# Kernel optimization log

Hardware: AMD Instinct MI355X
Metric: run time of the kernel (lower is better)

## Reference

```python
import jax, jax.numpy as jnp
import numpy as np

N = 100000   # nodes
E = 1600000  # edges
B = 64       # graphs
NI, EI, GI = 64, 32, 32   # node_in, edge_in, global_in
NO, EO, GO = 32, 32, 32   # node_out, edge_out, global_out
H = 3                     # attention heads
NEG_SLOPE = 0.2


def setup_inputs() -> dict:
    key = jax.random.key(0)
    ks = jax.random.split(key, 20)
    s = 0.1
    return {
        # graph data
        "x": jax.random.normal(ks[0], (N, NI), jnp.float32),
        "edge_attr": jax.random.normal(ks[1], (E, EI), jnp.float32),
        "glob": jax.random.normal(ks[2], (B, GI), jnp.float32),
        # edge_mlp: Lin(node_in+edge_in, edge_out)
        "W_edge": jax.random.normal(ks[3], (NI + EI, EO), jnp.float32) * s,
        "b_edge": jax.random.normal(ks[4], (EO,), jnp.float32) * s,
        # GATv2Conv params (heads=3, edge_dim=EO)
        "W_l": jax.random.normal(ks[5], (NI, H * NO), jnp.float32) * s,
        "b_l": jax.random.normal(ks[6], (H * NO,), jnp.float32) * s,
        "W_r": jax.random.normal(ks[7], (NI, H * NO), jnp.float32) * s,
        "b_r": jax.random.normal(ks[8], (H * NO,), jnp.float32) * s,
        "W_e": jax.random.normal(ks[9], (EO, H * NO), jnp.float32) * s,   # lin_edge (no bias)
        "att": jax.random.normal(ks[10], (H, NO), jnp.float32) * s,
        "bias_gat": jax.random.normal(ks[11], (H * NO,), jnp.float32) * s,
        # node_mlp_2: Lin(node_out*3 + global_in, node_out)
        "W_n2": jax.random.normal(ks[12], (H * NO + GI, NO), jnp.float32) * s,
        "b_n2": jax.random.normal(ks[13], (NO,), jnp.float32) * s,
        # global_mlp: Lin(global_in + node_out, global_out)
        "W_g": jax.random.normal(ks[14], (GI + NO, GO), jnp.float32) * s,
        "b_g": jax.random.normal(ks[15], (GO,), jnp.float32) * s,
        # int inputs
        "edge_index": jax.random.randint(ks[16], (2, E), 0, N, jnp.int32),
        "batch": jnp.sort(jax.random.randint(ks[17], (N,), 0, B, jnp.int32)),
    }


def reference(x, edge_attr, glob, W_edge, b_edge, W_l, b_l, W_r, b_r, W_e,
              att, bias_gat, W_n2, b_n2, W_g, b_g, edge_index, batch):
    src, dst = edge_index[0], edge_index[1]

    # --- edge model: relu(Lin([x[src], edge_attr])) ---
    e = jax.nn.relu(jnp.concatenate([x[src], edge_attr], axis=1) @ W_edge + b_edge)  # [E, EO]

    # --- node model: GATv2Conv(heads=3, edge_dim=EO), concat heads ---
    xl = (x @ W_l + b_l).reshape(N, H, NO)   # source transform
    xr = (x @ W_r + b_r).reshape(N, H, NO)   # target transform
    m = xl[src] + xr[dst] + (e @ W_e).reshape(E, H, NO)          # [E,H,NO]
    logits = (jax.nn.leaky_relu(m, NEG_SLOPE) * att).sum(-1)     # [E,H]
    # segment softmax over incoming edges of each target node
    mx = jax.ops.segment_max(logits, dst, num_segments=N)        # [N,H]
    ex = jnp.exp(logits - mx[dst])
    den = jax.ops.segment_sum(ex, dst, num_segments=N)           # [N,H]
    alpha = ex / den[dst]                                        # [E,H]
    msg = (alpha[..., None] * xl[src]).reshape(E, H * NO)
    gat_out = jax.ops.segment_sum(msg, dst, num_segments=N) + bias_gat  # [N, H*NO]
    x_new = jax.nn.relu(jnp.concatenate([gat_out, glob[batch]], axis=1) @ W_n2 + b_n2)  # [N,NO]

    # --- global model: relu(Lin([glob, scatter_mean(x_new, batch)])) ---
    cnt = jax.ops.segment_sum(jnp.ones((N,), x.dtype), batch, num_segments=B)
    mean = jax.ops.segment_sum(x_new, batch, num_segments=B) / jnp.maximum(cnt, 1.0)[:, None]
    u_new = jax.nn.relu(jnp.concatenate([glob, mean], axis=1) @ W_g + b_g)  # [B,GO]

    return x_new, e, u_new
```

## Files before the change

### kernel.cpp

```cpp
#include <hip/hip_runtime.h>

#define N_NODES 100000
#define N_EDGES 1600000
#define NB 64
#define NI 64
#define EI 32
#define GI 32
#define NO 32
#define EO 32
#define GO 32
#define HH 3
#define HNO 96
#define NEG 0.2f
#define SCAN_BLKS 98
#define SCAT_BLKS 1024
#define KE_BLKS 2048

__global__ __launch_bounds__(256) void kA_node(
    const float* __restrict__ x,
    const float* __restrict__ W_l, const float* __restrict__ b_l,
    const float* __restrict__ W_r, const float* __restrict__ b_r,
    const float* __restrict__ W_edge, const float* __restrict__ b_edge,
    float* __restrict__ xl, float* __restrict__ xr, float* __restrict__ pre_e,
    int niters)
{
    __shared__ float sWl[NI * HNO];
    __shared__ float sWr[NI * HNO];
    __shared__ float sWp[NI * 32];
    __shared__ float sx[64 * NI];
    int t = threadIdx.x;
    for (int f = t; f < NI * HNO; f += 256) { sWl[f] = W_l[f]; sWr[f] = W_r[f]; }
    for (int f = t; f < NI * 32; f += 256) sWp[f] = W_edge[f];
    __syncthreads();
    int k = t & 31, g = t >> 5;
    float bl0 = b_l[k], bl1 = b_l[k + 32], bl2 = b_l[k + 64];
    float br0 = b_r[k], br1 = b_r[k + 32], br2 = b_r[k + 64];
    float bpe = b_edge[k];
    const long NX = (long)N_NODES * NI;
    for (int it = 0; it < niters; ++it) {
        long nb = ((long)blockIdx.x + (long)it * gridDim.x) * 64;
        long base = nb * NI;
        for (int f = t; f < 64 * NI; f += 256) {
            long idx = base + f;
            sx[f] = x[idx < NX ? idx : 0];
        }
        __syncthreads();
        float aL0[8], aL1[8], aL2[8], aR0[8], aR1[8], aR2[8], aP[8];
        #pragma unroll
        for (int m = 0; m < 8; ++m) {
            aL0[m] = bl0; aL1[m] = bl1; aL2[m] = bl2;
            aR0[m] = br0; aR1[m] = br1; aR2[m] = br2;
            aP[m] = bpe;
        }
        const float* sxg = &sx[g * 8 * NI];
        for (int i = 0; i < NI; ++i) {
            float wl0 = sWl[i * HNO + k], wl1 = sWl[i * HNO + 32 + k], wl2 = sWl[i * HNO + 64 + k];
            float wr0 = sWr[i * HNO + k], wr1 = sWr[i * HNO + 32 + k], wr2 = sWr[i * HNO + 64 + k];
            float wp  = sWp[i * 32 + k];
            #pragma unroll
            for (int m = 0; m < 8; ++m) {
                float xv = sxg[m * NI + i];
                aL0[m] += xv * wl0; aL1[m] += xv * wl1; aL2[m] += xv * wl2;
                aR0[m] += xv * wr0; aR1[m] += xv * wr1; aR2[m] += xv * wr2;
                aP[m]  += xv * wp;
            }
        }
        #pragma unroll
        for (int m = 0; m < 8; ++m) {
            long n = nb + g * 8 + m;
            if (n < N_NODES) {
                xl[n * HNO + k]      = aL0[m];
                xl[n * HNO + 32 + k] = aL1[m];
                xl[n * HNO + 64 + k] = aL2[m];
                xr[n * HNO + k]      = aR0[m];
                xr[n * HNO + 32 + k] = aR1[m];
                xr[n * HNO + 64 + k] = aR2[m];
                pre_e[n * 32 + k]    = aP[m];
            }
        }
        __syncthreads();
    }
}

__global__ __launch_bounds__(256) void k_hist(const int* __restrict__ eidx, int* __restrict__ cnt)
{
    long i = (long)blockIdx.x * 256 + threadIdx.x;
    long stride = (long)gridDim.x * 256;
    for (; i < N_EDGES; i += stride)
        atomicAdd(&cnt[eidx[N_EDGES + i]], 1);
}

__global__ __launch_bounds__(1024) void k_scan1(const int* __restrict__ cnt, int* __restrict__ bsum)
{
    __shared__ int s[1024];
    int i = blockIdx.x * 1024 + threadIdx.x;
    s[threadIdx.x] = (i < N_NODES) ? cnt[i] : 0;
    for (int o = 512; o > 0; o >>= 1) {
        __syncthreads();
        if (threadIdx.x < o) s[threadIdx.x] += s[threadIdx.x + o];
    }
    if (threadIdx.x == 0) bsum[blockIdx.x] = s[0];
}

__global__ __launch_bounds__(128) void k_scan2(int* __restrict__ bsum)
{
    __shared__ int s[128];
    int v = (threadIdx.x < SCAN_BLKS) ? bsum[threadIdx.x] : 0;
    s[threadIdx.x] = v;
    for (int o = 1; o < 128; o <<= 1) {
        __syncthreads();
        int a = (threadIdx.x >= o) ? s[threadIdx.x - o] : 0;
        __syncthreads();
        s[threadIdx.x] += a;
    }
    if (threadIdx.x < SCAN_BLKS) bsum[threadIdx.x] = s[threadIdx.x] - v;
}

__global__ __launch_bounds__(1024) void k_scan3(const int* __restrict__ cnt,
                                                const int* __restrict__ bsum,
                                                int* __restrict__ off, int* __restrict__ cursor)
{
    __shared__ int s[1024];
    int i = blockIdx.x * 1024 + threadIdx.x;
    int v = (i < N_NODES) ? cnt[i] : 0;
    s[threadIdx.x] = v;
    for (int o = 1; o < 1024; o <<= 1) {
        __syncthreads();
        int a = (threadIdx.x >= o) ? s[threadIdx.x - o] : 0;
        __syncthreads();
        s[threadIdx.x] += a;
    }
    int excl = bsum[blockIdx.x] + s[threadIdx.x] - v;
    if (i < N_NODES) {
        off[i] = excl; cursor[i] = excl;
        if (i == N_NODES - 1) off[N_NODES] = excl + v;
    }
}

__global__ __launch_bounds__(256) void k_scat_ke(
    const int* __restrict__ eidx, int* __restrict__ cursor, int2* __restrict__ ep,
    const float* __restrict__ pre_e, const float* __restrict__ ea,
    const float* __restrict__ W_edge, float* __restrict__ e_out)
{
    __shared__ float sW2[32 * 32];
    __shared__ float sEa[8][32];
    int t = threadIdx.x;
    if (blockIdx.x < SCAT_BLKS) {
        long i = (long)blockIdx.x * 256 + t;
        long stride = (long)SCAT_BLKS * 256;
        for (; i < N_EDGES; i += stride) {
            int s = eidx[i];
            int d = eidx[N_EDGES + i];
            int pos = atomicAdd(&cursor[d], 1);
            ep[pos] = make_int2((int)i, s);
        }
    } else {
        int bid = blockIdx.x - SCAT_BLKS;
        for (int f = t; f < 32 * 32; f += 256) sW2[f] = W_edge[64 * 32 + f];
        __syncthreads();
        int k = t & 31, gid = t >> 5;
        const int niters = (N_EDGES + KE_BLKS * 8 - 1) / (KE_BLKS * 8);
        for (int it = 0; it < niters; ++it) {
            long e = ((long)bid + (long)it * KE_BLKS) * 8 + gid;
            bool valid = (e < N_EDGES);
            long ec = valid ? e : 0;
            int s = eidx[ec];
            float acc = pre_e[(long)s * 32 + k];
            sEa[gid][k] = ea[ec * EI + k];
            #pragma unroll 8
            for (int i = 0; i < 32; ++i) acc += sEa[gid][i] * sW2[i * 32 + k];
            if (valid) e_out[ec * EO + k] = fmaxf(acc, 0.f);
        }
    }
}

__global__ __launch_bounds__(256) void kF(
    const float* __restrict__ eo_in, const float* __restrict__ W_e,
    const float* __restrict__ att,
    const float* __restrict__ xl, const float* __restrict__ xr,
    const int2* __restrict__ ep, const int* __restrict__ off,
    const float* __restrict__ bias_gat,
    float* __restrict__ g_out, int niters)
{
    __shared__ float sWe[32 * 96];
    __shared__ float2 sEo2[8][32];
    int t = threadIdx.x;
    for (int f = t; f < 32 * 96; f += 256) sWe[f] = W_e[f];
    __syncthreads();
    int k = t & 31, gid = t >> 5;
    float at0 = att[k], at1 = att[32 + k], at2 = att[64 + k];
    float bg0 = bias_gat[k], bg1 = bias_gat[32 + k], bg2 = bias_gat[64 + k];
    for (int it = 0; it < niters; ++it) {
        long n = ((long)blockIdx.x + (long)it * gridDim.x) * 8 + gid;
        if (n >= N_NODES) continue;
        int lo = off[n], hi = off[n + 1];
        float xr0 = xr[n * HNO + k];
        float xr1 = xr[n * HNO + 32 + k];
        float xr2 = xr[n * HNO + 64 + k];
        float a0 = 0.f, a1 = 0.f, a2 = 0.f;
        float d0 = 0.f, d1 = 0.f, d2 = 0.f;
        int deg = hi - lo;
        int steps = (deg + 1) >> 1;
        int eA = 0, sA = 0, eB = 0, sB = 0;
        int eA1 = 0, sA1 = 0, eB1 = 0, sB1 = 0;
        float eoAc = 0.f, eoBc = 0.f;
        float xlA0 = 0.f, xlA1 = 0.f, xlA2 = 0.f, xlB0 = 0.f, xlB1 = 0.f, xlB2 = 0.f;
        if (steps > 0) {
            int2 q = ep[lo]; eA = q.x; sA = q.y;
            if (lo + 1 < hi) { int2 r = ep[lo + 1]; eB = r.x; sB = r.y; }
            eoAc = eo_in[(long)eA * EO + k];
            eoBc = eo_in[(long)eB * EO + k];
            xlA0 = xl[(long)sA * HNO + k]; xlA1 = xl[(long)sA * HNO + 32 + k]; xlA2 = xl[(long)sA * HNO + 64 + k];
            xlB0 = xl[(long)sB * HNO + k]; xlB1 = xl[(long)sB * HNO + 32 + k]; xlB2 = xl[(long)sB * HNO + 64 + k];
            if (lo + 2 < hi) { int2 q1 = ep[lo + 2]; eA1 = q1.x; sA1 = q1.y; }
            if (lo + 3 < hi) { int2 r1 = ep[lo + 3]; eB1 = r1.x; sB1 = r1.y; }
        }
        for (int st = 0; st < steps; ++st) {
            float eoA_n = eo_in[(long)eA1 * EO + k];
            float eoB_n = eo_in[(long)eB1 * EO + k];
            float xlA0n = xl[(long)sA1 * HNO + k], xlA1n = xl[(long)sA1 * HNO + 32 + k], xlA2n = xl[(long)sA1 * HNO + 64 + k];
            float xlB0n = xl[(long)sB1 * HNO + k], xlB1n = xl[(long)sB1 * HNO + 32 + k], xlB2n = xl[(long)sB1 * HNO + 64 + k];
            int eA2 = 0, sA2 = 0, eB2 = 0, sB2 = 0;
            int pA2 = lo + 2 * st + 4;
            if (pA2 < hi)     { int2 q2 = ep[pA2];     eA2 = q2.x; sA2 = q2.y; }
            if (pA2 + 1 < hi) { int2 r2 = ep[pA2 + 1]; eB2 = r2.x; sB2 = r2.y; }
            sEo2[gid][k] = make_float2(eoAc, eoBc);
            float hA0 = xlA0 + xr0, hA1 = xlA1 + xr1, hA2 = xlA2 + xr2;
            float hB0 = xlB0 + xr0, hB1 = xlB1 + xr1, hB2 = xlB2 + xr2;
            #pragma unroll 8
            for (int i = 0; i < 32; ++i) {
                float2 ov = sEo2[gid][i];
                float w0 = sWe[i * 96 + k], w1 = sWe[i * 96 + 32 + k], w2v = sWe[i * 96 + 64 + k];
                hA0 += ov.x * w0; hA1 += ov.x * w1; hA2 += ov.x * w2v;
                hB0 += ov.y * w0; hB1 += ov.y * w1; hB2 += ov.y * w2v;
            }
            float pA0 = (hA0 > 0.f ? hA0 : NEG * hA0) * at0;
            float pA1 = (hA1 > 0.f ? hA1 : NEG * hA1) * at1;
            float pA2v = (hA2 > 0.f ? hA2 : NEG * hA2) * at2;
            float pB0 = (hB0 > 0.f ? hB0 : NEG * hB0) * at0;
            float pB1 = (hB1 > 0.f ? hB1 : NEG * hB1) * at1;
            float pB2 = (hB2 > 0.f ? hB2 : NEG * hB2) * at2;
            #pragma unroll
            for (int m = 1; m <= 16; m <<= 1) {
                pA0 += __shfl_xor(pA0, m, 32); pA1 += __shfl_xor(pA1, m, 32); pA2v += __shfl_xor(pA2v, m, 32);
                pB0 += __shfl_xor(pB0, m, 32); pB1 += __shfl_xor(pB1, m, 32); pB2 += __shfl_xor(pB2, m, 32);
            }
            bool okB = (lo + 2 * st + 1) < hi;
            float exA0 = __expf(pA0), exA1 = __expf(pA1), exA2 = __expf(pA2v);
            float exB0 = 0.f, exB1 = 0.f, exB2 = 0.f;
            if (okB) { exB0 = __expf(pB0); exB1 = __expf(pB1); exB2 = __expf(pB2); }
            a0 += exA0 * xlA0; a1 += exA1 * xlA1; a2 += exA2 * xlA2;
            a0 += exB0 * xlB0; a1 += exB1 * xlB1; a2 += exB2 * xlB2;
            d0 += exA0 + exB0; d1 += exA1 + exB1; d2 += exA2 + exB2;
            eA = eA1; sA = sA1; eB = eB1; sB = sB1;
            eA1 = eA2; sA1 = sA2; eB1 = eB2; sB1 = sB2;
            eoAc = eoA_n; eoBc = eoB_n;
            xlA0 = xlA0n; xlA1 = xlA1n; xlA2 = xlA2n;
            xlB0 = xlB0n; xlB1 = xlB1n; xlB2 = xlB2n;
        }
        g_out[n * HNO + k]      = (d0 > 0.f ? a0 / d0 : 0.f) + bg0;
        g_out[n * HNO + 32 + k] = (d1 > 0.f ? a1 / d1 : 0.f) + bg1;
        g_out[n * HNO + 64 + k] = (d2 > 0.f ? a2 / d2 : 0.f) + bg2;
    }
}

__global__ __launch_bounds__(256) void k2_node_out(
    const float* __restrict__ g, const float* __restrict__ glob,
    const int* __restrict__ batch, const float* __restrict__ W_n2,
    const float* __restrict__ b_n2, float* __restrict__ x_new, int niters)
{
    __shared__ float sW[128 * 32];
    __shared__ float sIn[8][128];
    int t = threadIdx.x;
    for (int f = t; f < 128 * 32; f += 256) sW[f] = W_n2[f];
    __syncthreads();
    int k = t & 31, ni = t >> 5;
    float bn = b_n2[k];
    for (int it = 0; it < niters; ++it) {
        long n = ((long)blockIdx.x + (long)it * gridDim.x) * 8 + ni;
        long nc = (n < N_NODES) ? n : 0;
        #pragma unroll
        for (int r = 0; r < 3; ++r) {
            int j = r * 32 + k;
            sIn[ni][j] = g[nc * HNO + j];
        }
        sIn[ni][96 + k] = glob[(long)batch[nc] * GI + k];
        __syncthreads();
        float acc = bn;
        #pragma unroll 8
        for (int i = 0; i < 128; ++i) acc += sIn[ni][i] * sW[i * 32 + k];
        if (n < N_NODES) x_new[n * NO + k] = fmaxf(acc, 0.f);
        __syncthreads();
    }
}

__device__ __forceinline__ int lower_bound_dev(const int* __restrict__ a, int n, int v) {
    int lo = 0, hi = n;
    while (lo < hi) { int mid = (lo + hi) >> 1; if (a[mid] < v) lo = mid + 1; else hi = mid; }
    return lo;
}

__global__ __launch_bounds__(256) void k3_global(
    const float* __restrict__ x_new, const int* __restrict__ batch,
    const float* __restrict__ glob, const float* __restrict__ W_g,
    const float* __restrict__ b_g, float* __restrict__ u_new)
{
    __shared__ int s_lo, s_hi;
    __shared__ float s_part[8][32];
    __shared__ float s_mean[32];
    int g = blockIdx.x;
    if (threadIdx.x == 0) {
        s_lo = lower_bound_dev(batch, N_NODES, g);
        s_hi = lower_bound_dev(batch, N_NODES, g + 1);
    }
    __syncthreads();
    int lo = s_lo, hi = s_hi;
    int k = threadIdx.x & 31, c = threadIdx.x >> 5;
    float acc = 0.f;
    for (long n = lo + c; n < hi; n += 8) acc += x_new[n * NO + k];
    s_part[c][k] = acc;
    __syncthreads();
    if (threadIdx.x < 32) {
        float s = 0.f;
        #pragma unroll
        for (int c2 = 0; c2 < 8; ++c2) s += s_part[c2][k];
        int cnt = hi - lo;
        s_mean[k] = s / (float)(cnt > 0 ? cnt : 1);
    }
    __syncthreads();
    if (threadIdx.x < 32) {
        float acc2 = b_g[k];
        #pragma unroll
        for (int i = 0; i < 32; ++i) acc2 += glob[g * GI + i] * W_g[i * GO + k];
        #pragma unroll
        for (int i = 0; i < 32; ++i) acc2 += s_mean[i] * W_g[(32 + i) * GO + k];
        u_new[g * GO + k] = fmaxf(acc2, 0.f);
    }
}

extern "C" void kernel_launch(void* const* d_in, const int* in_sizes, int n_in,
                              void* d_out, int out_size, void* d_ws, size_t ws_size,
                              hipStream_t stream) {
    const float* x        = (const float*)d_in[0];
    const float* edge_attr= (const float*)d_in[1];
    const float* glob     = (const float*)d_in[2];
    const float* W_edge   = (const float*)d_in[3];
    const float* b_edge   = (const float*)d_in[4];
    const float* W_l      = (const float*)d_in[5];
    const float* b_l      = (const float*)d_in[6];
    const float* W_r      = (const float*)d_in[7];
    const float* b_r      = (const float*)d_in[8];
    const float* W_e      = (const float*)d_in[9];
    const float* att      = (const float*)d_in[10];
    const float* bias_gat = (const float*)d_in[11];
    const float* W_n2     = (const float*)d_in[12];
    const float* b_n2     = (const float*)d_in[13];
    const float* W_g      = (const float*)d_in[14];
    const float* b_g      = (const float*)d_in[15];
    const int* edge_index = (const int*)d_in[16];
    const int* batch      = (const int*)d_in[17];

    float* out   = (float*)d_out;
    float* x_new = out;
    float* e_out = out + (size_t)N_NODES * NO;
    float* u_new = e_out + (size_t)N_EDGES * EO;

    float*  ws    = (float*)d_ws;
    float*  xl    = ws;
    float*  xr    = xl + (size_t)N_NODES * HNO;
    float*  pre_e = xr + (size_t)N_NODES * HNO;
    float*  g_buf = pre_e + (size_t)N_NODES * 32;
    int2*   ep    = (int2*)(g_buf + (size_t)N_NODES * HNO);
    int*    cnt   = (int*)(ep + (size_t)N_EDGES);
    int*    off   = cnt + N_NODES;
    int*    cursor= off + N_NODES + 1;
    int*    bsum  = cursor + N_NODES;

    hipMemsetAsync(cnt, 0, (size_t)N_NODES * sizeof(int), stream);

    k_hist<<<1024, 256, 0, stream>>>(edge_index, cnt);
    k_scan1<<<SCAN_BLKS, 1024, 0, stream>>>(cnt, bsum);
    k_scan2<<<1, 128, 0, stream>>>(bsum);
    k_scan3<<<SCAN_BLKS, 1024, 0, stream>>>(cnt, bsum, off, cursor);

    int gridA = 1024;
    int groups64 = (N_NODES + 63) / 64;
    int itA = (groups64 + gridA - 1) / gridA;
    kA_node<<<gridA, 256, 0, stream>>>(x, W_l, b_l, W_r, b_r, W_edge, b_edge,
                                       xl, xr, pre_e, itA);

    k_scat_ke<<<SCAT_BLKS + KE_BLKS, 256, 0, stream>>>(edge_index, cursor, ep,
                                                       pre_e, edge_attr, W_edge, e_out);

    int gridF = 2048;
    int groups8 = (N_NODES + 7) / 8;
    int itF = (groups8 + gridF - 1) / gridF;
    kF<<<gridF, 256, 0, stream>>>(e_out, W_e, att, xl, xr,
                                  ep, off, bias_gat, g_buf, itF);

    int grid2 = 1024;
    int it2 = (groups8 + grid2 - 1) / grid2;
    k2_node_out<<<grid2, 256, 0, stream>>>(g_buf, glob, batch, W_n2, b_n2, x_new, it2);

    k3_global<<<NB, 256, 0, stream>>>(x_new, batch, glob, W_g, b_g, u_new);
}
```

Measured before the change: 1.343 ms.

## Interleave head dimension in xl/xr/W_e and split scatter from edge MLP kernel

Stores xl and xr with the three heads interleaved per output column, so each lane reads its three head values from adjacent addresses. The W_e shared-memory copy is permuted to match. The edge-index scatter becomes its own kernel instead of sharing blocks with the edge-MLP. The edge-MLP now processes two edges per warp group to reuse each weight read from shared memory. The aim is fewer gather instructions and better weight reuse. The cost is losing the overlap between scatter and edge compute, and strided per-lane access that may not vectorize cleanly.

Result: faster. 1.286 ms (-4.3%).

```diff
diff --git a/kernel.cpp b/kernel.cpp
--- a/kernel.cpp
+++ b/kernel.cpp
@@ -13,15 +13,13 @@
 #define HNO 96
 #define NEG 0.2f
 #define SCAN_BLKS 98
-#define SCAT_BLKS 1024
-#define KE_BLKS 2048
 
 __global__ __launch_bounds__(256) void kA_node(
     const float* __restrict__ x,
     const float* __restrict__ W_l, const float* __restrict__ b_l,
     const float* __restrict__ W_r, const float* __restrict__ b_r,
     const float* __restrict__ W_edge, const float* __restrict__ b_edge,
-    float* __restrict__ xl, float* __restrict__ xr, float* __restrict__ pre_e,
+    float* __restrict__ xl3, float* __restrict__ xr3, float* __restrict__ pre_e,
     int niters)
 {
     __shared__ float sWl[NI * HNO];
@@ -69,13 +67,14 @@
         for (int m = 0; m < 8; ++m) {
             long n = nb + g * 8 + m;
             if (n < N_NODES) {
-                xl[n * HNO + k]      = aL0[m];
-                xl[n * HNO + 32 + k] = aL1[m];
-                xl[n * HNO + 64 + k] = aL2[m];
-                xr[n * HNO + k]      = aR0[m];
-                xr[n * HNO + 32 + k] = aR1[m];
-                xr[n * HNO + 64 + k] = aR2[m];
-                pre_e[n * 32 + k]    = aP[m];
+                long b3 = n * HNO + (long)k * 3;
+                xl3[b3]     = aL0[m];
+                xl3[b3 + 1] = aL1[m];
+                xl3[b3 + 2] = aL2[m];
+                xr3[b3]     = aR0[m];
+                xr3[b3 + 1] = aR1[m];
+                xr3[b3 + 2] = aR2[m];
+                pre_e[n * 32 + k] = aP[m];
             }
         }
         __syncthreads();
@@ -137,66 +136,78 @@
     }
 }
 
-__global__ __launch_bounds__(256) void k_scat_ke(
-    const int* __restrict__ eidx, int* __restrict__ cursor, int2* __restrict__ ep,
-    const float* __restrict__ pre_e, const float* __restrict__ ea,
-    const float* __restrict__ W_edge, float* __restrict__ e_out)
+__global__ __launch_bounds__(256) void k_scatter(const int* __restrict__ eidx,
+                                                 int* __restrict__ cursor,
+                                                 int2* __restrict__ ep)
+{
+    long i = (long)blockIdx.x * 256 + threadIdx.x;
+    long stride = (long)gridDim.x * 256;
+    for (; i < N_EDGES; i += stride) {
+        int s = eidx[i];
+        int d = eidx[N_EDGES + i];
+        int pos = atomicAdd(&cursor[d], 1);
+        ep[pos] = make_int2((int)i, s);
+    }
+}
+
+__global__ __launch_bounds__(256) void kE_edge(
+    const int* __restrict__ eidx, const float* __restrict__ pre_e,
+    const float* __restrict__ ea, const float* __restrict__ W_edge,
+    float* __restrict__ e_out, int niters)
 {
     __shared__ float sW2[32 * 32];
-    __shared__ float sEa[8][32];
+    __shared__ float2 sEa2[8][32];
     int t = threadIdx.x;
-    if (blockIdx.x < SCAT_BLKS) {
-        long i = (long)blockIdx.x * 256 + t;
-        long stride = (long)SCAT_BLKS * 256;
-        for (; i < N_EDGES; i += stride) {
-            int s = eidx[i];
-            int d = eidx[N_EDGES + i];
-            int pos = atomicAdd(&cursor[d], 1);
-            ep[pos] = make_int2((int)i, s);
-        }
-    } else {
-        int bid = blockIdx.x - SCAT_BLKS;
-        for (int f = t; f < 32 * 32; f += 256) sW2[f] = W_edge[64 * 32 + f];
-        __syncthreads();
-        int k = t & 31, gid = t >> 5;
-        const int niters = (N_EDGES + KE_BLKS * 8 - 1) / (KE_BLKS * 8);
-        for (int it = 0; it < niters; ++it) {
-            long e = ((long)bid + (long)it * KE_BLKS) * 8 + gid;
-            bool valid = (e < N_EDGES);
-            long ec = valid ? e : 0;
-            int s = eidx[ec];
-            float acc = pre_e[(long)s * 32 + k];
-            sEa[gid][k] = ea[ec * EI + k];
-            #pragma unroll 8
-            for (int i = 0; i < 32; ++i) acc += sEa[gid][i] * sW2[i * 32 + k];
-            if (valid) e_out[ec * EO + k] = fmaxf(acc, 0.f);
-        }
+    for (int f = t; f < 32 * 32; f += 256) sW2[f] = W_edge[64 * 32 + f];
+    __syncthreads();
+    int k = t & 31, gid = t >> 5;
+    for (int it = 0; it < niters; ++it) {
+        long e0 = ((long)blockIdx.x + (long)it * gridDim.x) * 16 + gid * 2;
+        long e1 = e0 + 1;
+        bool v0 = (e0 < N_EDGES), v1 = (e1 < N_EDGES);
+        long c0 = v0 ? e0 : 0, c1 = v1 ? e1 : 0;
+        int s0 = eidx[c0], s1 = eidx[c1];
+        float acc0 = pre_e[(long)s0 * 32 + k];
+        float acc1 = pre_e[(long)s1 * 32 + k];
+        sEa2[gid][k] = make_float2(ea[c0 * EI + k], ea[c1 * EI + k]);
+        #pragma unroll 8
+        for (int i = 0; i < 32; ++i) {
+            float w = sW2[i * 32 + k];
+            float2 v = sEa2[gid][i];
+            acc0 += v.x * w; acc1 += v.y * w;
+        }
+        if (v0) e_out[c0 * EO + k] = fmaxf(acc0, 0.f);
+        if (v1) e_out[c1 * EO + k] = fmaxf(acc1, 0.f);
     }
 }
 
 __global__ __launch_bounds__(256) void kF(
     const float* __restrict__ eo_in, const float* __restrict__ W_e,
     const float* __restrict__ att,
-    const float* __restrict__ xl, const float* __restrict__ xr,
+    const float* __restrict__ xl3, const float* __restrict__ xr3,
     const int2* __restrict__ ep, const int* __restrict__ off,
     const float* __restrict__ bias_gat,
     float* __restrict__ g_out, int niters)
 {
-    __shared__ float sWe[32 * 96];
+    __shared__ float sWeI[32 * 96];
     __shared__ float2 sEo2[8][32];
     int t = threadIdx.x;
-    for (int f = t; f < 32 * 96; f += 256) sWe[f] = W_e[f];
+    for (int f = t; f < 32 * 96; f += 256) {
+        int i = f / 96, r = f - i * 96;
+        int kk = r / 3, h = r - kk * 3;
+        sWeI[f] = W_e[i * 96 + h * 32 + kk];
+    }
     __syncthreads();
     int k = t & 31, gid = t >> 5;
     float at0 = att[k], at1 = att[32 + k], at2 = att[64 + k];
     float bg0 = bias_gat[k], bg1 = bias_gat[32 + k], bg2 = bias_gat[64 + k];
+    const int k3 = k * 3;
     for (int it = 0; it < niters; ++it) {
         long n = ((long)blockIdx.x + (long)it * gridDim.x) * 8 + gid;
         if (n >= N_NODES) continue;
         int lo = off[n], hi = off[n + 1];
-        float xr0 = xr[n * HNO + k];
-        float xr1 = xr[n * HNO + 32 + k];
-        float xr2 = xr[n * HNO + 64 + k];
+        long nb3 = n * HNO + k3;
+        float xr0 = xr3[nb3], xr1 = xr3[nb3 + 1], xr2 = xr3[nb3 + 2];
         float a0 = 0.f, a1 = 0.f, a2 = 0.f;
         float d0 = 0.f, d1 = 0.f, d2 = 0.f;
         int deg = hi - lo;
@@ -210,16 +221,18 @@
             if (lo + 1 < hi) { int2 r = ep[lo + 1]; eB = r.x; sB = r.y; }
             eoAc = eo_in[(long)eA * EO + k];
             eoBc = eo_in[(long)eB * EO + k];
-            xlA0 = xl[(long)sA * HNO + k]; xlA1 = xl[(long)sA * HNO + 32 + k]; xlA2 = xl[(long)sA * HNO + 64 + k];
-            xlB0 = xl[(long)sB * HNO + k]; xlB1 = xl[(long)sB * HNO + 32 + k]; xlB2 = xl[(long)sB * HNO + 64 + k];
+            long a3 = (long)sA * HNO + k3, b3 = (long)sB * HNO + k3;
+            xlA0 = xl3[a3]; xlA1 = xl3[a3 + 1]; xlA2 = xl3[a3 + 2];
+            xlB0 = xl3[b3]; xlB1 = xl3[b3 + 1]; xlB2 = xl3[b3 + 2];
             if (lo + 2 < hi) { int2 q1 = ep[lo + 2]; eA1 = q1.x; sA1 = q1.y; }
             if (lo + 3 < hi) { int2 r1 = ep[lo + 3]; eB1 = r1.x; sB1 = r1.y; }
         }
         for (int st = 0; st < steps; ++st) {
             float eoA_n = eo_in[(long)eA1 * EO + k];
             float eoB_n = eo_in[(long)eB1 * EO + k];
-            float xlA0n = xl[(long)sA1 * HNO + k], xlA1n = xl[(long)sA1 * HNO + 32 + k], xlA2n = xl[(long)sA1 * HNO + 64 + k];
-            float xlB0n = xl[(long)sB1 * HNO + k], xlB1n = xl[(long)sB1 * HNO + 32 + k], xlB2n = xl[(long)sB1 * HNO + 64 + k];
+            long a3 = (long)sA1 * HNO + k3, b3 = (long)sB1 * HNO + k3;
+            float xlA0n = xl3[a3], xlA1n = xl3[a3 + 1], xlA2n = xl3[a3 + 2];
+            float xlB0n = xl3[b3], xlB1n = xl3[b3 + 1], xlB2n = xl3[b3 + 2];
             int eA2 = 0, sA2 = 0, eB2 = 0, sB2 = 0;
             int pA2 = lo + 2 * st + 4;
             if (pA2 < hi)     { int2 q2 = ep[pA2];     eA2 = q2.x; sA2 = q2.y; }
@@ -230,7 +243,8 @@
             #pragma unroll 8
             for (int i = 0; i < 32; ++i) {
                 float2 ov = sEo2[gid][i];
-                float w0 = sWe[i * 96 + k], w1 = sWe[i * 96 + 32 + k], w2v = sWe[i * 96 + 64 + k];
+                const float* wp = &sWeI[i * 96 + k3];
+                float w0 = wp[0], w1 = wp[1], w2v = wp[2];
                 hA0 += ov.x * w0; hA1 += ov.x * w1; hA2 += ov.x * w2v;
                 hB0 += ov.y * w0; hB1 += ov.y * w1; hB2 += ov.y * w2v;
             }
@@ -366,9 +380,9 @@
     float* u_new = e_out + (size_t)N_EDGES * EO;
 
     float*  ws    = (float*)d_ws;
-    float*  xl    = ws;
-    float*  xr    = xl + (size_t)N_NODES * HNO;
-    float*  pre_e = xr + (size_t)N_NODES * HNO;
+    float*  xl3   = ws;
+    float*  xr3   = xl3 + (size_t)N_NODES * HNO;
+    float*  pre_e = xr3 + (size_t)N_NODES * HNO;
     float*  g_buf = pre_e + (size_t)N_NODES * 32;
     int2*   ep    = (int2*)(g_buf + (size_t)N_NODES * HNO);
     int*    cnt   = (int*)(ep + (size_t)N_EDGES);
@@ -382,20 +396,23 @@
     k_scan1<<<SCAN_BLKS, 1024, 0, stream>>>(cnt, bsum);
     k_scan2<<<1, 128, 0, stream>>>(bsum);
     k_scan3<<<SCAN_BLKS, 1024, 0, stream>>>(cnt, bsum, off, cursor);
+    k_scatter<<<1024, 256, 0, stream>>>(edge_index, cursor, ep);
 
     int gridA = 1024;
     int groups64 = (N_NODES + 63) / 64;
     int itA = (groups64 + gridA - 1) / gridA;
     kA_node<<<gridA, 256, 0, stream>>>(x, W_l, b_l, W_r, b_r, W_edge, b_edge,
-                                       xl, xr, pre_e, itA);
-
-    k_scat_ke<<<SCAT_BLKS + KE_BLKS, 256, 0, stream>>>(edge_index, cursor, ep,
-                                                       pre_e, edge_attr, W_edge, e_out);
+                                       xl3, xr3, pre_e, itA);
+
+    int gridE = 2048;
+    int groupsE = (N_EDGES + 15) / 16;
+    int itE = (groupsE + gridE - 1) / gridE;
+    kE_edge<<<gridE, 256, 0, stream>>>(edge_index, pre_e, edge_attr, W_edge, e_out, itE);
 
     int gridF = 2048;
     int groups8 = (N_NODES + 7) / 8;
     int itF = (groups8 + gridF - 1) / gridF;
-    kF<<<gridF, 256, 0, stream>>>(e_out, W_e, att, xl, xr,
+    kF<<<gridF, 256, 0, stream>>>(e_out, W_e, att, xl3, xr3,
                                   ep, off, bias_gat, g_buf, itF);
 
     int grid2 = 1024;
```
